# Kernel optimization log

Hardware: AMD Instinct MI355X
Metric: run time of the kernel (lower is better)

The kernel has to match this reference:

```python
import jax, jax.numpy as jnp
import numpy as np

B, T, N, CIN = 8, 12, 883, 3
C, E, H = 64, 10, 8
HD = C // H
TOPK = 48  # int(5 * log2(883))
DIL = [1, 2, 1, 2, 1, 2, 1, 2]
NEG = -9.0e15
L = 8

def _l2norm(v, ax):
    return v / jnp.maximum(jnp.linalg.norm(v, axis=ax, keepdims=True), 1e-12)

def _gelu(v):
    return jax.nn.gelu(v, approximate=False)

def setup_inputs():
    key = jax.random.key(0)
    ks = list(jax.random.split(key, 48))
    it = iter(ks)
    ch0 = jax.random.normal(next(it), (B, T, N))
    ch1 = jax.random.uniform(next(it), (B, T, N))                    # time-of-day in [0,1)
    ch2 = jax.random.randint(next(it), (B, T, N), 0, 7).astype(jnp.float32)  # day-of-week
    x = jnp.stack([ch0, ch1, ch2], axis=-1)
    def row_norm(kk):
        a = jax.random.uniform(kk, (N, N))
        return a / a.sum(axis=1, keepdims=True)
    def w(kk, shape):
        fan_in = shape[-2] if len(shape) >= 2 else shape[-1]
        return (jax.random.normal(kk, shape) * (1.0 / float(np.sqrt(fan_in)))).astype(jnp.float32)
    inp = dict(
        x=x,
        support0=row_norm(next(it)),
        support1=row_norm(next(it)),
        TiD=jax.random.normal(next(it), (288, E)) * 0.1,
        DiW=jax.random.normal(next(it), (7, E)) * 0.1,
        E1=jax.random.normal(next(it), (N, E)) * 0.1,
        E2=jax.random.normal(next(it), (N, E)) * 0.1,
        E3=jax.random.normal(next(it), (N, E)) * 0.1,
        Wx=w(next(it), (T // 2 + 1, E)),
        Wd=w(next(it), (N, 4 * E, E)),
        Wxabs=w(next(it), (E, E)),
        start_w=w(next(it), (CIN, C)), start_b=jnp.zeros((C,)),
        Wq=w(next(it), (L, C, C)), bq=jnp.zeros((L, C)),
        Wk=w(next(it), (L, C, C)), bk=jnp.zeros((L, C)),
        Wv=w(next(it), (L, C, C)), bv=jnp.zeros((L, C)),
        W1=w(next(it), (L, C, 4 * C)), b1=jnp.zeros((L, 4 * C)),
        W2=w(next(it), (L, 4 * C, C)), b2=jnp.zeros((L, C)),
        filt_w=jax.random.normal(next(it), (L, 2, C, C)) * (1.0 / float(np.sqrt(2 * C))),
        filt_b=jnp.zeros((L, C)),
        gate_w=jax.random.normal(next(it), (L, 2, C, C)) * (1.0 / float(np.sqrt(2 * C))),
        gate_b=jnp.zeros((L, C)),
        skip_w=w(next(it), (L, C, 256)), skip_b=jnp.zeros((L, 256)),
        gcn_w=w(next(it), (L, 9 * C, C)), gcn_b=jnp.zeros((L, C)),
        bn_g=jnp.ones((L, C)), bn_b=jnp.zeros((L, C)),
        end1_w=w(next(it), (256, 512)), end1_b=jnp.zeros((512,)),
        end2_w=w(next(it), (512, T)), end2_b=jnp.zeros((T,)),
    )
    return inp

def _graph_gen(xs, T_D, D_W, E3, Wx, Wd, Wxabs):
    # xs: [B,T,N] raw signal channel
    xf = jnp.abs(jnp.fft.rfft(xs, axis=1))                 # [B,F=7,N]
    xf = _l2norm(_l2norm(xf, 1), 2)
    xe = jnp.einsum('btn,td->bnd', xf, Wx)                 # [B,N,E]
    e3 = jnp.broadcast_to(E3[None], (xe.shape[0], N, E))
    xcat = jnp.concatenate([xe, e3, T_D, D_W], axis=2)     # [B,N,4E]
    x1 = jax.nn.relu(jnp.einsum('bnf,nfe->bne', xcat, Wd)) # per-node weight
    mu = x1.mean(axis=(1, 2), keepdims=True)               # LayerNorm over [N,E]
    var = ((x1 - mu) ** 2).mean(axis=(1, 2), keepdims=True)
    x1k = (x1 - mu) / jnp.sqrt(var + 1e-8)
    dew = jnp.einsum('bne,ek->bnk', x1k, Wxabs)
    adp = jax.nn.relu(jnp.einsum('bnk,bmk->bnm', dew, x1)) # [B,N,N]
    _, idx = jax.lax.top_k(adp, TOPK)                      # [B,N,K] per-row topk
    bi = jnp.arange(adp.shape[0])[:, None, None]
    ri = jnp.arange(N)[None, :, None]
    mask = jnp.zeros_like(adp).at[bi, ri, idx].set(1.0)
    return jax.nn.softmax(adp * mask, axis=2)

def reference(x, support0, support1, TiD, DiW, E1, E2, E3, Wx, Wd, Wxabs,
              start_w, start_b, Wq, bq, Wk, bk, Wv, bv, W1, b1, W2, b2,
              filt_w, filt_b, gate_w, gate_b, skip_w, skip_b,
              gcn_w, gcn_b, bn_g, bn_b, end1_w, end1_b, end2_w, end2_b):
    tid = (x[:, -1, :, 1] * 288).astype(jnp.int32)         # [B,N]
    T_D = TiD[tid]                                         # [B,N,E]
    D_W = DiW[x[:, -1, :, 2].astype(jnp.int32)]
    Adap = jax.nn.softmax(jax.nn.relu(E1 @ E2.T), axis=1)
    AD = _graph_gen(x[..., 0], T_D, D_W, E3, Wx, Wd, Wxabs)
    supports = [support0, support1, Adap, AD]

    h = jnp.transpose(x, (0, 3, 2, 1))                     # [B,3,N,T]
    h = jnp.pad(h, ((0, 0), (0, 0), (0, 0), (1, 0)))       # pad to receptive_field=13
    h = jnp.einsum('io,bint->bont', start_w, h) + start_b[None, :, None, None]

    skip = None
    for l in range(L):
        res = h
        # --- causal temporal attention ---
        Xa = jnp.transpose(h, (0, 3, 2, 1))                # [B,Tc,N,C]
        Tc = Xa.shape[1]
        q = _gelu(Xa @ Wq[l] + bq[l]).reshape(-1, Tc, N, H, HD)
        k = _gelu(Xa @ Wk[l] + bk[l]).reshape(-1, Tc, N, H, HD)
        v = _gelu(Xa @ Wv[l] + bv[l]).reshape(-1, Tc, N, H, HD)
        att = jnp.einsum('btnhd,bsnhd->bnhts', q, k) / (HD ** 0.5)
        cmask = jnp.tril(jnp.ones((Tc, Tc), bool))
        att = jax.nn.softmax(jnp.where(cmask, att, NEG), axis=-1)
        o = jnp.einsum('bnhts,bsnhd->bnthd', att, v).reshape(-1, N, Tc, C)
        o = _gelu(o @ W1[l] + b1[l]) @ W2[l] + b2[l]
        h = jnp.transpose(o, (0, 3, 1, 2)) + res           # [B,C,N,Tc]
        # --- gated dilated causal conv (kernel (1,2), dilation d) ---
        d = DIL[l]
        a0, a1 = h[..., :-d], h[..., d:]
        f = jnp.tanh(jnp.einsum('io,bint->bont', filt_w[l, 0], a0)
                     + jnp.einsum('io,bint->bont', filt_w[l, 1], a1)
                     + filt_b[l][None, :, None, None])
        g = jax.nn.sigmoid(jnp.einsum('io,bint->bont', gate_w[l, 0], a0)
                           + jnp.einsum('io,bint->bont', gate_w[l, 1], a1)
                           + gate_b[l][None, :, None, None])
        h = f * g
        s = jnp.einsum('io,bint->bont', skip_w[l], h) + skip_b[l][None, :, None, None]
        skip = s if skip is None else s + skip[..., -s.shape[3]:]
        # --- diffusion graph conv, order 2 over 4 supports ---
        out = [h]
        for a in supports:
            if a.ndim == 3:
                x1 = jnp.einsum('bcvt,bwv->bcwt', h, a)
                x2 = jnp.einsum('bcvt,bwv->bcwt', x1, a)
            else:
                x1 = jnp.einsum('bcvt,vw->bcwt', h, a)
                x2 = jnp.einsum('bcvt,vw->bcwt', x1, a)
            out += [x1, x2]
        hc = jnp.concatenate(out, axis=1)                  # [B,9C,N,Tc']
        h = jnp.einsum('io,bint->bont', gcn_w[l], hc) + gcn_b[l][None, :, None, None]
        h = h + res[..., -h.shape[3]:]
        # --- BatchNorm2d (batch statistics, training-mode normalization) ---
        mu = h.mean(axis=(0, 2, 3), keepdims=True)
        var = ((h - mu) ** 2).mean(axis=(0, 2, 3), keepdims=True)
        h = bn_g[l][None, :, None, None] * (h - mu) / jnp.sqrt(var + 1e-5) \
            + bn_b[l][None, :, None, None]

    out = jax.nn.relu(skip)
    out = jax.nn.relu(jnp.einsum('io,bint->bont', end1_w, out)
                      + end1_b[None, :, None, None])
    out = jnp.einsum('io,bint->bont', end2_w, out) + end2_b[None, :, None, None]
    return out  # [B, out_steps=12, N, 1]
```

## Files before the change

kernel.cpp:

```cpp
#include <hip/hip_runtime.h>
#include <math.h>

#define DIVUP(a,b) (((a)+(b)-1)/(b))

namespace {

constexpr int B=8, T=12, N=883, CIN=3, C=64, E=10, H=8, HD=8, TOPK=48, L=8;
constexpr int SKC=256, F7=7, T13=13;
constexpr int NP=896;

typedef __attribute__((ext_vector_type(8))) short bf16x8;
typedef __attribute__((ext_vector_type(4))) float f32x4;

__device__ __forceinline__ float geluf(float x){ return 0.5f*x*(1.0f+erff(x*0.7071067811865475f)); }
__device__ __forceinline__ float sigmf(float x){ return 1.0f/(1.0f+expf(-x)); }
__device__ __forceinline__ float us2f(unsigned short u){ return __uint_as_float(((unsigned)u)<<16); }
__device__ __forceinline__ unsigned short f2us(float f){
  unsigned x=__float_as_uint(f);
  return (unsigned short)((x + 0x7fffu + ((x>>16)&1u))>>16);
}

template<int KK, int STRIDE, int KW>
__device__ __forceinline__ f32x4 tile_mm(
    const unsigned short* sAh, const unsigned short* sAl,
    const unsigned short* __restrict__ Wh, const unsigned short* __restrict__ Wl,
    int colBase, int lane, f32x4 acc){
  int lr=lane&15, lg=lane>>4;
  #pragma unroll
  for(int k0=0;k0<KK;k0+=32){
    bf16x8 ah=*(const bf16x8*)&sAh[lr*STRIDE+k0+8*lg];
    bf16x8 al=*(const bf16x8*)&sAl[lr*STRIDE+k0+8*lg];
    bf16x8 bh=*(const bf16x8*)&Wh[(size_t)(colBase+lr)*KW+k0+8*lg];
    bf16x8 bl=*(const bf16x8*)&Wl[(size_t)(colBase+lr)*KW+k0+8*lg];
    acc=__builtin_amdgcn_mfma_f32_16x16x32_bf16(ah,bh,acc,0,0,0);
    acc=__builtin_amdgcn_mfma_f32_16x16x32_bf16(ah,bl,acc,0,0,0);
    acc=__builtin_amdgcn_mfma_f32_16x16x32_bf16(al,bh,acc,0,0,0);
  }
  return acc;
}

__global__ void k_dft(const float* __restrict__ x, float* __restrict__ xf){
  int idx = blockIdx.x*256 + threadIdx.x;
  if(idx >= B*F7*N) return;
  int n = idx % N; int f = (idx/N) % F7; int b = idx/(N*F7);
  float re=0.f, im=0.f;
  for(int t=0;t<T;t++){
    float v = x[((size_t)(b*T+t)*N+n)*CIN];
    float ang = -6.283185307179586f * (float)(f*t) / 12.0f;
    re += v*cosf(ang); im += v*sinf(ang);
  }
  xf[idx] = sqrtf(re*re+im*im);
}

__global__ void k_l2f(float* __restrict__ xf){
  int idx = blockIdx.x*256 + threadIdx.x;
  if(idx >= B*N) return;
  int n = idx % N; int b = idx / N;
  float s=0.f;
  for(int f=0;f<F7;f++){ float v=xf[((size_t)b*F7+f)*N+n]; s+=v*v; }
  float inv = 1.0f/fmaxf(sqrtf(s), 1e-12f);
  for(int f=0;f<F7;f++) xf[((size_t)b*F7+f)*N+n] *= inv;
}

__global__ void k_l2n(float* __restrict__ xf){
  int bf = blockIdx.x; int tid = threadIdx.x;
  __shared__ float red[256];
  size_t base = (size_t)bf*N;
  float s=0.f;
  for(int i=tid;i<N;i+=256){ float v=xf[base+i]; s+=v*v; }
  red[tid]=s; __syncthreads();
  for(int k=128;k>0;k>>=1){ if(tid<k) red[tid]+=red[tid+k]; __syncthreads(); }
  float inv = 1.0f/fmaxf(sqrtf(red[0]), 1e-12f);
  __syncthreads();
  for(int i=tid;i<N;i+=256) xf[base+i]*=inv;
}

__global__ void k_x1(const float* __restrict__ x, const float* __restrict__ xf,
                     const float* __restrict__ E3, const float* __restrict__ TiD,
                     const float* __restrict__ DiW, const float* __restrict__ Wx,
                     const float* __restrict__ Wd, float* __restrict__ x1){
  int idx = blockIdx.x*256+threadIdx.x;
  if(idx>=B*N) return;
  int n=idx%N, b=idx/N;
  float xc[40];
  for(int d=0;d<E;d++){
    float a=0.f;
    for(int f=0;f<F7;f++) a += xf[((size_t)b*F7+f)*N+n]*Wx[f*E+d];
    xc[d]=a;
  }
  for(int d=0;d<E;d++) xc[10+d]=E3[n*E+d];
  int ti = (int)(x[((size_t)(b*T+(T-1))*N+n)*CIN+1]*288.0f);
  int dw = (int)(x[((size_t)(b*T+(T-1))*N+n)*CIN+2]);
  for(int d=0;d<E;d++) xc[20+d]=TiD[ti*E+d];
  for(int d=0;d<E;d++) xc[30+d]=DiW[dw*E+d];
  for(int e=0;e<E;e++){
    float a=0.f;
    for(int f=0;f<40;f++) a += xc[f]*Wd[((size_t)n*40+f)*E+e];
    x1[(size_t)idx*E+e]=fmaxf(a,0.f);
  }
}

__global__ void k_lnstats(const float* __restrict__ x1, float* __restrict__ st){
  int b=blockIdx.x, tid=threadIdx.x;
  __shared__ float rs[256], rq[256];
  const int M=N*E;
  float s=0.f,q=0.f;
  for(int i=tid;i<M;i+=256){ float v=x1[(size_t)b*M+i]; s+=v; q+=v*v; }
  rs[tid]=s; rq[tid]=q; __syncthreads();
  for(int k=128;k>0;k>>=1){ if(tid<k){ rs[tid]+=rs[tid+k]; rq[tid]+=rq[tid+k]; } __syncthreads(); }
  if(tid==0){ float mu=rs[0]/M; float var=rq[0]/M-mu*mu; st[b*2]=mu; st[b*2+1]=var; }
}

__global__ void k_dew(const float* __restrict__ x1, const float* __restrict__ st,
                      const float* __restrict__ Wxabs, float* __restrict__ dew){
  int idx=blockIdx.x*256+threadIdx.x;
  if(idx>=B*N) return;
  int b=idx/N;
  float mu=st[b*2], var=st[b*2+1];
  float rs=rsqrtf(var+1e-8f);
  float xk[E];
  for(int e=0;e<E;e++) xk[e]=(x1[(size_t)idx*E+e]-mu)*rs;
  for(int k=0;k<E;k++){
    float a=0.f;
    for(int e=0;e<E;e++) a+=xk[e]*Wxabs[e*E+k];
    dew[(size_t)idx*E+k]=a;
  }
}

__global__ void k_adp(const float* __restrict__ dew, const float* __restrict__ x1,
                      float* __restrict__ adp){
  size_t idx=(size_t)blockIdx.x*256+threadIdx.x;
  if(idx>=(size_t)B*N*N) return;
  int m=(int)(idx%N); int n=(int)((idx/N)%N); int b=(int)(idx/((size_t)N*N));
  const float* dr=dew+((size_t)b*N+n)*E;
  const float* xr=x1+((size_t)b*N+m)*E;
  float a=0.f;
  for(int k=0;k<E;k++) a+=dr[k]*xr[k];
  adp[idx]=fmaxf(a,0.f);
}

__global__ __launch_bounds__(256) void k_topk(const float* __restrict__ adp,
                       unsigned short* __restrict__ ADhi, unsigned short* __restrict__ ADlo){
  int row = blockIdx.x*4 + (threadIdx.x>>6);
  int lane = threadIdx.x & 63;
  const float* rp = adp + (size_t)row*N;
  float v[14];
  #pragma unroll
  for(int j=0;j<14;j++){
    int i = lane + j*64;
    v[j] = (i<N) ? rp[i] : -1.f;
  }
  unsigned sel = 0u;
  float m0 = 0.f;
  for(int k=0;k<TOPK;k++){
    float bv = -2.f; int bi = 1<<20;
    #pragma unroll
    for(int j=0;j<14;j++){
      if(!((sel>>j)&1u) && v[j] > bv){ bv = v[j]; bi = lane + j*64; }
    }
    #pragma unroll
    for(int off=1; off<64; off<<=1){
      float ov = __shfl_xor(bv, off);
      int   oi = __shfl_xor(bi, off);
      if(ov > bv || (ov==bv && oi<bi)){ bv=ov; bi=oi; }
    }
    if(k==0) m0 = bv;
    if((bi&63)==lane) sel |= 1u << (bi>>6);
  }
  float pv[14];
  float ls = 0.f;
  #pragma unroll
  for(int j=0;j<14;j++){
    int i = lane + j*64;
    float p = ((sel>>j)&1u) ? v[j] : 0.f;
    pv[j] = p;
    if(i<N) ls += expf(p - m0);
  }
  #pragma unroll
  for(int off=1; off<64; off<<=1) ls += __shfl_xor(ls, off);
  float invZ = 1.f/ls;
  size_t base = ((size_t)(row/N)*NP + (size_t)(row%N))*NP;
  #pragma unroll
  for(int j=0;j<14;j++){
    int i = lane + j*64;
    if(i<N){
      float f = expf(pv[j]-m0)*invZ;
      unsigned short h=f2us(f);
      ADhi[base+i]=h; ADlo[base+i]=f2us(f-us2f(h));
    }
  }
}

__global__ void k_adap(const float* __restrict__ E1, const float* __restrict__ E2,
                       unsigned short* __restrict__ Mh, unsigned short* __restrict__ Ml){
  int v=blockIdx.x, tid=threadIdx.x;
  __shared__ float rowv[N];
  __shared__ float rv[256];
  float e1[E];
  for(int e=0;e<E;e++) e1[e]=E1[v*E+e];
  for(int j=tid;j<N;j+=256){
    float s=0.f;
    for(int e=0;e<E;e++) s+=e1[e]*E2[j*E+e];
    rowv[j]=fmaxf(s,0.f);
  }
  __syncthreads();
  float lm=-1e30f;
  for(int j=tid;j<N;j+=256) lm=fmaxf(lm,rowv[j]);
  rv[tid]=lm; __syncthreads();
  for(int s=128;s>0;s>>=1){ if(tid<s) rv[tid]=fmaxf(rv[tid],rv[tid+s]); __syncthreads(); }
  float m=rv[0]; __syncthreads();
  float ls=0.f;
  for(int j=tid;j<N;j+=256) ls+=expf(rowv[j]-m);
  rv[tid]=ls; __syncthreads();
  for(int s=128;s>0;s>>=1){ if(tid<s) rv[tid]+=rv[tid+s]; __syncthreads(); }
  float invZ=1.0f/rv[0];
  for(int j=tid;j<N;j+=256){
    float f=expf(rowv[j]-m)*invZ;
    unsigned short h=f2us(f);
    Mh[(size_t)j*NP+v]=h; Ml[(size_t)j*NP+v]=f2us(f-us2f(h));
  }
}

__global__ void k_cvtT(const float* __restrict__ A, unsigned short* __restrict__ Mh,
                       unsigned short* __restrict__ Ml){
  int idx=blockIdx.x*256+threadIdx.x;
  if(idx>=N*N) return;
  int w=idx/N, v=idx%N;
  float f=A[(size_t)v*N+w];
  unsigned short h=f2us(f);
  Mh[(size_t)w*NP+v]=h;
  Ml[(size_t)w*NP+v]=f2us(f-us2f(h));
}

__global__ void k_cvt_qkv(const float* __restrict__ Wq, const float* __restrict__ Wk,
                          const float* __restrict__ Wv,
                          unsigned short* __restrict__ dh, unsigned short* __restrict__ dl){
  int idx=blockIdx.x*256+threadIdx.x;
  if(idx>=L*192*64) return;
  int l=idx/12288, rem=idx%12288, col=rem/64, k=rem%64;
  int mat=col>>6, o=col&63;
  const float* W=(mat==0)?Wq:((mat==1)?Wk:Wv);
  float v=W[(size_t)l*4096 + k*64 + o];
  unsigned short h=f2us(v);
  dh[idx]=h; dl[idx]=f2us(v-us2f(h));
}
__global__ void k_cvt_w1(const float* __restrict__ W1,
                         unsigned short* __restrict__ dh, unsigned short* __restrict__ dl){
  int idx=blockIdx.x*256+threadIdx.x;
  if(idx>=L*256*64) return;
  int l=idx/16384, rem=idx%16384, col=rem/64, k=rem%64;
  float v=W1[(size_t)l*16384 + k*256 + col];
  unsigned short h=f2us(v);
  dh[idx]=h; dl[idx]=f2us(v-us2f(h));
}
__global__ void k_cvt_w2(const float* __restrict__ W2,
                         unsigned short* __restrict__ dh, unsigned short* __restrict__ dl){
  int idx=blockIdx.x*256+threadIdx.x;
  if(idx>=L*64*256) return;
  int l=idx/16384, rem=idx%16384, col=rem/256, k=rem%256;
  float v=W2[(size_t)l*16384 + k*64 + col];
  unsigned short h=f2us(v);
  dh[idx]=h; dl[idx]=f2us(v-us2f(h));
}
__global__ void k_cvt_conv(const float* __restrict__ fw, const float* __restrict__ gw,
                           unsigned short* __restrict__ dh, unsigned short* __restrict__ dl){
  int idx=blockIdx.x*256+threadIdx.x;
  if(idx>=L*128*128) return;
  int l=idx/16384, rem=idx%16384, col=rem/128, k=rem%128;
  int c=col&63, fg=col>>6, tap=k>>6, i=k&63;
  const float* W=fg?gw:fw;
  float v=W[(size_t)l*8192 + tap*4096 + i*64 + c];
  unsigned short h=f2us(v);
  dh[idx]=h; dl[idx]=f2us(v-us2f(h));
}
__global__ void k_cvt_gcn(const float* __restrict__ Wg,
                          unsigned short* __restrict__ dh, unsigned short* __restrict__ dl){
  int idx=blockIdx.x*256+threadIdx.x;
  if(idx>=L*64*576) return;
  int l=idx/36864, rem=idx%36864, o=rem/576, k=rem%576;
  float v=Wg[((size_t)l*576 + k)*64 + o];
  unsigned short h=f2us(v);
  dh[idx]=h; dl[idx]=f2us(v-us2f(h));
}

__global__ void k_zero(float* __restrict__ p, int n){
  int idx=blockIdx.x*256+threadIdx.x;
  if(idx<n) p[idx]=0.f;
}
__global__ void k_zeroUS(unsigned short* __restrict__ p, long long n){
  long long idx=(long long)blockIdx.x*256+threadIdx.x;
  if(idx<n) p[idx]=0;
}

__global__ __launch_bounds__(256) void k_trx(
    const unsigned short* __restrict__ Sh, const unsigned short* __restrict__ Sl,
    unsigned short* __restrict__ Dh, unsigned short* __restrict__ Dl, int M){
  __shared__ unsigned short th[64][66], tl[64][66];
  int b=blockIdx.z;
  int m0=blockIdx.x*64, n0=blockIdx.y*64;
  int tid=threadIdx.x;
  const unsigned short* sbh=Sh + (size_t)b*N*M;
  const unsigned short* sbl=Sl + (size_t)b*N*M;
  for(int idx=tid; idx<64*64; idx+=256){
    int i=idx>>6, j=idx&63;
    int n=n0+i;
    unsigned short vh=0, vl=0;
    if(n<N){
      size_t o=(size_t)n*M + m0+j;
      vh=sbh[o]; vl=sbl[o];
    }
    th[j][i]=vh; tl[j][i]=vl;
  }
  __syncthreads();
  unsigned short* dbh=Dh + (size_t)b*M*NP;
  unsigned short* dbl=Dl + (size_t)b*M*NP;
  for(int idx=tid; idx<64*64; idx+=256){
    int r=idx>>6, cc=idx&63;
    size_t o=(size_t)(m0+r)*NP + n0+cc;
    dbh[o]=th[r][cc]; dbl[o]=tl[r][cc];
  }
}

__global__ void k_start(const float* __restrict__ x, const float* __restrict__ sw,
                        const float* __restrict__ sb, float* __restrict__ h){
  int idx=blockIdx.x*256+threadIdx.x;
  if(idx>=B*N*T13*C) return;
  int c=idx&63; int t=(idx>>6)%T13; int n=(idx/(64*T13))%N; int b=idx/(64*T13*N);
  float a=sb[c];
  if(t>0){
    size_t xb=((size_t)(b*T+(t-1))*N+n)*CIN;
    for(int i=0;i<CIN;i++) a += sw[i*C+c]*x[xb+i];
  }
  h[idx]=a;
}

template<int TC, int D>
__global__ __launch_bounds__(256) void k_attconv(const float* __restrict__ hin,
  const unsigned short* __restrict__ Wqkvh, const unsigned short* __restrict__ Wqkvl,
  const unsigned short* __restrict__ W1h,   const unsigned short* __restrict__ W1l,
  const unsigned short* __restrict__ W2h,   const unsigned short* __restrict__ W2l,
  const unsigned short* __restrict__ Wch,   const unsigned short* __restrict__ Wcl,
  const float* __restrict__ bq, const float* __restrict__ bk, const float* __restrict__ bv,
  const float* __restrict__ b1, const float* __restrict__ b2,
  const float* __restrict__ fb, const float* __restrict__ gb,
  const float* __restrict__ skw, const float* __restrict__ skb,
  unsigned short* __restrict__ hThi, unsigned short* __restrict__ hTlo,
  float* __restrict__ skipacc){
  constexpr int TN = TC - D;
  int bn=blockIdx.x; int tid=threadIdx.x;
  int n=bn%N, b=bn/N;
  int lane=tid&63, wid=tid>>6;
  int lr=lane&15, lg=lane>>4;
  __shared__ __align__(16) float sxa[16*64];
  __shared__ __align__(16) float sq [16*64];
  __shared__ __align__(16) float sk [16*64];
  __shared__ __align__(16) float sv [16*64];
  __shared__ __align__(16) unsigned short sA1h[16*72], sA1l[16*72];
  __shared__ __align__(16) unsigned short sA2h[16*264], sA2l[16*264];
  __shared__ __align__(16) float sfg[16*128];

  const float* hp = hin + (size_t)bn*TC*64;
  for(int idx=tid; idx<TC*64; idx+=256){
    int t=idx>>6, c=idx&63;
    float v=hp[idx];
    sxa[idx]=v;
    unsigned short h=f2us(v);
    sA1h[t*72+c]=h; sA1l[t*72+c]=f2us(v-us2f(h));
  }
  for(int idx=tid; idx<(16-TC)*64; idx+=256){
    int t=TC+(idx>>6), c=idx&63;
    sxa[t*64+c]=0.f; sA1h[t*72+c]=0; sA1l[t*72+c]=0;
  }
  __syncthreads();

  #pragma unroll
  for(int it=0; it<3; ++it){
    int tile=it*4+wid;
    f32x4 acc={0.f,0.f,0.f,0.f};
    acc=tile_mm<64,72,64>(sA1h,sA1l,Wqkvh,Wqkvl,tile*16,lane,acc);
    int col=tile*16+lr; int mat=col>>6, o=col&63;
    const float* bm=(mat==0)?bq:((mat==1)?bk:bv);
    float* dst=(mat==0)?sq:((mat==1)?sk:sv);
    float bias=bm[o];
    #pragma unroll
    for(int r=0;r<4;r++){
      int t=lg*4+r;
      if(t<TC) dst[t*64+o]=geluf(acc[r]+bias);
    }
  }
  __syncthreads();

  if(tid<H*TC){
    int hh=tid/TC, t=tid%TC;
    const float* qr=&sq[t*64+hh*HD];
    float att[TC];
    float m=-1e30f;
    #pragma unroll
    for(int s=0;s<TC;s++){
      float a=0.f;
      #pragma unroll
      for(int d=0;d<HD;d++) a+=qr[d]*sk[s*64+hh*HD+d];
      a*=0.3535533905932738f;
      a=(s<=t)?a:-1e30f;
      att[s]=a; m=fmaxf(m,a);
    }
    float Z=0.f;
    #pragma unroll
    for(int s=0;s<TC;s++){ float e=expf(att[s]-m); att[s]=e; Z+=e; }
    float invZ=1.0f/Z;
    #pragma unroll
    for(int d=0;d<HD;d++){
      float o=0.f;
      #pragma unroll
      for(int s=0;s<TC;s++) o+=att[s]*sv[s*64+hh*HD+d];
      float v=o*invZ;
      unsigned short h=f2us(v);
      sA1h[t*72+hh*8+d]=h; sA1l[t*72+hh*8+d]=f2us(v-us2f(h));
    }
  }
  __syncthreads();

  #pragma unroll
  for(int it=0; it<4; ++it){
    int tile=it*4+wid;
    f32x4 acc={0.f,0.f,0.f,0.f};
    acc=tile_mm<64,72,64>(sA1h,sA1l,W1h,W1l,tile*16,lane,acc);
    int col=tile*16+lr;
    float bias=b1[col];
    #pragma unroll
    for(int r=0;r<4;r++){
      int t=lg*4+r;
      float v=(t<TC)?geluf(acc[r]+bias):0.f;
      unsigned short h=f2us(v);
      sA2h[t*264+col]=h; sA2l[t*264+col]=f2us(v-us2f(h));
    }
  }
  __syncthreads();

  {
    int tile=wid;
    f32x4 acc={0.f,0.f,0.f,0.f};
    acc=tile_mm<256,264,256>(sA2h,sA2l,W2h,W2l,tile*16,lane,acc);
    int col=tile*16+lr;
    float bias=b2[col];
    #pragma unroll
    for(int r=0;r<4;r++){
      int t=lg*4+r;
      if(t<TC) sq[t*64+col]=acc[r]+bias+sxa[t*64+col];
    }
  }
  __syncthreads();

  for(int idx=tid; idx<16*128; idx+=256){
    int t=idx>>7, k=idx&127;
    int c=k&63;
    float v=0.f;
    if(t<TN) v=sq[((k<64)?t:(t+D))*64+c];
    unsigned short h=f2us(v);
    sA2h[t*136+k]=h; sA2l[t*136+k]=f2us(v-us2f(h));
  }
  __syncthreads();

  #pragma unroll
  for(int it=0; it<2; ++it){
    int tile=it*4+wid;
    f32x4 acc={0.f,0.f,0.f,0.f};
    acc=tile_mm<128,136,128>(sA2h,sA2l,Wch,Wcl,tile*16,lane,acc);
    int col=tile*16+lr;
    float bias=(col<64)?fb[col]:gb[col&63];
    #pragma unroll
    for(int r=0;r<4;r++){
      int t=lg*4+r;
      float v=acc[r]+bias;
      sfg[t*128+col]=(col<64)?tanhf(v):sigmf(v);
    }
  }
  __syncthreads();

  if(tid<C) sk[tid]=sfg[(TN-1)*128+tid]*sfg[(TN-1)*128+64+tid];
  __syncthreads();

  {
    float a=skb[tid];
    for(int i=0;i<C;i++) a+=sk[i]*skw[i*SKC+tid];
    skipacc[((size_t)b*SKC+tid)*N+n]+=a;
  }
  size_t obase=(size_t)bn*64*TN;
  for(int idx=tid; idx<TN*64; idx+=256){
    int tt=idx>>6, c=idx&63;
    float v=sfg[tt*128+c]*sfg[tt*128+64+c];
    unsigned short h=f2us(v);
    hThi[obase+idx]=h;
    hTlo[obase+idx]=f2us(v-us2f(h));
  }
}

__global__ __launch_bounds__(256) void k_spatmm(
    const unsigned short* __restrict__ Ah, const unsigned short* __restrict__ Al,
    long long aStride,
    const unsigned short* __restrict__ Xh, const unsigned short* __restrict__ Xl,
    const unsigned short* __restrict__ XTh, const unsigned short* __restrict__ XTl,
    int xT,
    unsigned short* __restrict__ Yh, unsigned short* __restrict__ Yl,
    unsigned short* __restrict__ YTh, unsigned short* __restrict__ YTl,
    int M){
  __shared__ unsigned short sAh[64*40];
  __shared__ unsigned short sAl[64*40];
  __shared__ unsigned short sXh[64*40];
  __shared__ unsigned short sXl[64*40];
  int b=blockIdx.z;
  const unsigned short* Abh=Ah+(size_t)b*aStride;
  const unsigned short* Abl=Al+(size_t)b*aStride;
  int tid=threadIdx.x;
  int w0=blockIdx.x*64, c0=blockIdx.y*64;
  int lane=tid&63, wid=tid>>6;
  int wr=wid>>1, wc=wid&1;
  int lr=lane&15, lg=lane>>4;
  f32x4 acc[2][2];
  #pragma unroll
  for(int j=0;j<2;j++){
    #pragma unroll
    for(int i=0;i<2;i++){ acc[j][i][0]=0.f; acc[j][i][1]=0.f; acc[j][i][2]=0.f; acc[j][i][3]=0.f; }
  }
  const int ar=tid>>2, akb=(tid&3)*8;
  const int xk=tid>>3, xcb=(tid&7)*8;
  const int xkx=xk ^ (8*((xcb>>3)&3));
  for(int k0=0;k0<N;k0+=32){
    {
      uint4 qh=*(const uint4*)&Abh[(size_t)(w0+ar)*NP + k0+akb];
      uint4 ql=*(const uint4*)&Abl[(size_t)(w0+ar)*NP + k0+akb];
      *(uint4*)&sAh[ar*40+akb]=qh;
      *(uint4*)&sAl[ar*40+akb]=ql;
    }
    if(xT){
      const unsigned short* Xbth=XTh+(size_t)b*M*NP;
      const unsigned short* Xbtl=XTl+(size_t)b*M*NP;
      uint4 qh=*(const uint4*)&Xbth[(size_t)(c0+ar)*NP + k0+akb];
      uint4 ql=*(const uint4*)&Xbtl[(size_t)(c0+ar)*NP + k0+akb];
      *(uint4*)&sXh[ar*40+akb]=qh;
      *(uint4*)&sXl[ar*40+akb]=ql;
    }else{
      const unsigned short* Xbh=Xh+(size_t)b*N*M;
      const unsigned short* Xbl=Xl+(size_t)b*N*M;
      uint4 qh={0,0,0,0}, ql={0,0,0,0};
      if(k0+xk<N){
        qh=*(const uint4*)&Xbh[(size_t)(k0+xk)*M + c0+xcb];
        ql=*(const uint4*)&Xbl[(size_t)(k0+xk)*M + c0+xcb];
      }
      unsigned short uh[8], ul[8];
      uh[0]=(unsigned short)(qh.x&0xffff); uh[1]=(unsigned short)(qh.x>>16);
      uh[2]=(unsigned short)(qh.y&0xffff); uh[3]=(unsigned short)(qh.y>>16);
      uh[4]=(unsigned short)(qh.z&0xffff); uh[5]=(unsigned short)(qh.z>>16);
      uh[6]=(unsigned short)(qh.w&0xffff); uh[7]=(unsigned short)(qh.w>>16);
      ul[0]=(unsigned short)(ql.x&0xffff); ul[1]=(unsigned short)(ql.x>>16);
      ul[2]=(unsigned short)(ql.y&0xffff); ul[3]=(unsigned short)(ql.y>>16);
      ul[4]=(unsigned short)(ql.z&0xffff); ul[5]=(unsigned short)(ql.z>>16);
      ul[6]=(unsigned short)(ql.w&0xffff); ul[7]=(unsigned short)(ql.w>>16);
      #pragma unroll
      for(int j=0;j<8;j++){
        sXh[(xcb+j)*40+xkx]=uh[j];
        sXl[(xcb+j)*40+xkx]=ul[j];
      }
    }
    __syncthreads();
    bf16x8 a_h[2], a_l[2], x_h[2], x_l[2];
    #pragma unroll
    for(int j=0;j<2;j++){
      int r=32*wr+16*j+lr;
      a_h[j]=*(const bf16x8*)&sAh[r*40+8*lg];
      a_l[j]=*(const bf16x8*)&sAl[r*40+8*lg];
    }
    #pragma unroll
    for(int i=0;i<2;i++){
      int cc=32*wc+16*i+lr;
      int g = xT ? lg : (lg ^ ((cc>>3)&3));
      x_h[i]=*(const bf16x8*)&sXh[cc*40+8*g];
      x_l[i]=*(const bf16x8*)&sXl[cc*40+8*g];
    }
    #pragma unroll
    for(int j=0;j<2;j++){
      #pragma unroll
      for(int i=0;i<2;i++){
        acc[j][i]=__builtin_amdgcn_mfma_f32_16x16x32_bf16(a_h[j],x_h[i],acc[j][i],0,0,0);
        acc[j][i]=__builtin_amdgcn_mfma_f32_16x16x32_bf16(a_h[j],x_l[i],acc[j][i],0,0,0);
        acc[j][i]=__builtin_amdgcn_mfma_f32_16x16x32_bf16(a_l[j],x_h[i],acc[j][i],0,0,0);
      }
    }
    __syncthreads();
  }
  #pragma unroll
  for(int j=0;j<2;j++){
    int rbase=w0+32*wr+16*j+lg*4;
    #pragma unroll
    for(int i=0;i<2;i++){
      int col=c0+32*wc+16*i+lr;
      unsigned short hh[4], ll[4];
      #pragma unroll
      for(int r=0;r<4;r++){
        float v=acc[j][i][r];
        hh[r]=f2us(v);
        ll[r]=f2us(v-us2f(hh[r]));
      }
      #pragma unroll
      for(int r=0;r<4;r++){
        int row=rbase+r;
        if(row<N){
          size_t o=((size_t)b*N+row)*M+col;
          Yh[o]=hh[r]; Yl[o]=ll[r];
        }
      }
      if(YTh){
        size_t o=(size_t)b*M*NP + (size_t)col*NP + rbase;
        ushort4 ph; ph.x=hh[0]; ph.y=hh[1]; ph.z=hh[2]; ph.w=hh[3];
        ushort4 pl; pl.x=ll[0]; pl.y=ll[1]; pl.z=ll[2]; pl.w=ll[3];
        *(ushort4*)&YTh[o]=ph;
        *(ushort4*)&YTl[o]=pl;
      }
    }
  }
}

template<int TN, int FIRST>
__global__ __launch_bounds__(256) void k_gcnmm(
    const unsigned short* __restrict__ S0h, const unsigned short* __restrict__ S0l,
    const unsigned short* __restrict__ S1h, const unsigned short* __restrict__ S1l,
    const unsigned short* __restrict__ S2h, const unsigned short* __restrict__ S2l,
    const unsigned short* __restrict__ Wbh, const unsigned short* __restrict__ Wbl,
    int kOff,
    const float* __restrict__ gb, const float* __restrict__ res,
    float* __restrict__ acc, int Tc){
  constexpr int SL=64*TN;
  constexpr int NS=FIRST?3:2;
  constexpr int KK=NS*64;
  __shared__ unsigned short sAh[64*40], sAl[64*40];
  int bn0=blockIdx.x*4;
  int tid=threadIdx.x, lane=tid&63, wid=tid>>6;
  int lr=lane&15, lg=lane>>4;
  f32x4 a4[4];
  #pragma unroll
  for(int rt=0;rt<4;rt++){ a4[rt][0]=0.f; a4[rt][1]=0.f; a4[rt][2]=0.f; a4[rt][3]=0.f; }
  const int ar=tid>>2, akb=(tid&3)*8;
  const int ani=ar>>4, att_=ar&15;
  #pragma unroll
  for(int kc=0; kc<KK/32; ++kc){
    int k0=kc*32; int j=k0>>6; int i0=k0&63;
    const unsigned short* sh=(j==0)?S0h:((j==1)?S1h:S2h);
    const unsigned short* sl=(j==0)?S0l:((j==1)?S1l:S2l);
    uint4 qh={0,0,0,0}, ql={0,0,0,0};
    if(att_<TN){
      size_t o=(size_t)(bn0+ani)*SL + att_*64 + i0 + akb;
      qh=*(const uint4*)&sh[o]; ql=*(const uint4*)&sl[o];
    }
    *(uint4*)&sAh[ar*40+akb]=qh;
    *(uint4*)&sAl[ar*40+akb]=ql;
    __syncthreads();
    bf16x8 bh=*(const bf16x8*)&Wbh[(size_t)(wid*16+lr)*576 + kOff + k0 + 8*lg];
    bf16x8 bl=*(const bf16x8*)&Wbl[(size_t)(wid*16+lr)*576 + kOff + k0 + 8*lg];
    #pragma unroll
    for(int rt=0;rt<4;rt++){
      bf16x8 ah=*(const bf16x8*)&sAh[(rt*16+lr)*40+8*lg];
      bf16x8 al=*(const bf16x8*)&sAl[(rt*16+lr)*40+8*lg];
      a4[rt]=__builtin_amdgcn_mfma_f32_16x16x32_bf16(ah,bh,a4[rt],0,0,0);
      a4[rt]=__builtin_amdgcn_mfma_f32_16x16x32_bf16(ah,bl,a4[rt],0,0,0);
      a4[rt]=__builtin_amdgcn_mfma_f32_16x16x32_bf16(al,bh,a4[rt],0,0,0);
    }
    __syncthreads();
  }
  int o=wid*16+lr;
  #pragma unroll
  for(int rt=0;rt<4;rt++){
    int bn=bn0+rt;
    #pragma unroll
    for(int r=0;r<4;r++){
      int t2=lg*4+r;
      if(t2<TN){
        size_t oi=((size_t)bn*TN + t2)*64 + o;
        float v=a4[rt][r];
        if(FIRST){
          v += gb[o] + res[((size_t)bn*Tc + (Tc-TN) + t2)*64 + o];
          acc[oi]=v;
        }else{
          acc[oi]+=v;
        }
      }
    }
  }
}

__global__ __launch_bounds__(256) void k_bnstats1(const float* __restrict__ h,
                                                  float* __restrict__ part, int R){
  int tid=threadIdx.x;
  int c=tid&63, rg=tid>>6;
  float s=0.f,q=0.f;
  for(int r=blockIdx.x*4+rg; r<R; r+=1024){
    float v=h[(size_t)r*64+c];
    s+=v; q+=v*v;
  }
  __shared__ float ls[256], lq[256];
  ls[tid]=s; lq[tid]=q; __syncthreads();
  if(rg==0){
    s=ls[c]+ls[64+c]+ls[128+c]+ls[192+c];
    q=lq[c]+lq[64+c]+lq[128+c]+lq[192+c];
    part[blockIdx.x*128+c]=s;
    part[blockIdx.x*128+64+c]=q;
  }
}
__global__ __launch_bounds__(256) void k_bnstats2(const float* __restrict__ part,
                                                  float* __restrict__ st, int R){
  int tid=threadIdx.x;
  int c=tid&63, g=tid>>6;
  float s=0.f,q=0.f;
  for(int p=g;p<256;p+=4){ s+=part[p*128+c]; q+=part[p*128+64+c]; }
  __shared__ float ls[256], lq[256];
  ls[tid]=s; lq[tid]=q; __syncthreads();
  if(g==0){
    s=ls[c]+ls[64+c]+ls[128+c]+ls[192+c];
    q=lq[c]+lq[64+c]+lq[128+c]+lq[192+c];
    float mu=s/R;
    float var=q/R-mu*mu;
    st[c]=mu; st[64+c]=rsqrtf(var+1e-5f);
  }
}

__global__ void k_bnapply(float* __restrict__ h, const float* __restrict__ st,
                          const float* __restrict__ g, const float* __restrict__ bb, int total){
  int idx=blockIdx.x*256+threadIdx.x;
  if(idx>=total) return;
  int c=idx&63;
  float v=h[idx];
  h[idx]=(v-st[c])*st[64+c]*g[c]+bb[c];
}

__global__ void k_head(const float* __restrict__ skipacc, const float* __restrict__ W1,
  const float* __restrict__ b1, const float* __restrict__ W2, const float* __restrict__ b2,
  float* __restrict__ out){
  int gid=blockIdx.x; int tid=threadIdx.x;
  int n=gid%N; int b=gid/N;
  __shared__ float s[SKC];
  __shared__ float hid[512];
  if(tid<SKC){
    float v=skipacc[((size_t)b*SKC+tid)*N+n];
    s[tid]=fmaxf(v,0.f);
  }
  __syncthreads();
  {
    float a=b1[tid];
    for(int i=0;i<SKC;i++) a+=s[i]*W1[(size_t)i*512+tid];
    hid[tid]=fmaxf(a,0.f);
  }
  __syncthreads();
  if(tid<T){
    float a=b2[tid];
    for(int j=0;j<512;j++) a+=hid[j]*W2[(size_t)j*T+tid];
    out[((size_t)b*T+tid)*N+n]=a;
  }
}

struct Ctx {
  const float *bq,*bk,*bv,*b1,*b2,*filt_b,*gate_b,*skip_w,*skip_b,*gcn_b,*bn_g,*bn_b;
  const unsigned short *qkvTh,*qkvTl,*w1Th,*w1Tl,*w2Th,*w2Tl,*cvTh,*cvTl,*wgh,*wgl;
  const unsigned short* matH[4];
  const unsigned short* matL[4];
  long long matStride[4];
  float *pH,*pAlt,*skipacc,*bnst,*bnpart;
  unsigned short *hThi,*hTlo,*Phi,*Plo,*Qhi,*Qlo;
  unsigned short *hTth,*hTtl,*PTh,*PTl;
  hipStream_t stream;
};

template<int TC, int D>
void run_layer(Ctx& c, int l, bool last){
  constexpr int TN=TC-D;
  k_attconv<TC,D><<<B*N,256,0,c.stream>>>(c.pH,
    c.qkvTh+(size_t)l*12288, c.qkvTl+(size_t)l*12288,
    c.w1Th+(size_t)l*16384,  c.w1Tl+(size_t)l*16384,
    c.w2Th+(size_t)l*16384,  c.w2Tl+(size_t)l*16384,
    c.cvTh+(size_t)l*16384,  c.cvTl+(size_t)l*16384,
    c.bq+(size_t)l*C, c.bk+(size_t)l*C, c.bv+(size_t)l*C,
    c.b1+(size_t)l*4*C, c.b2+(size_t)l*C,
    c.filt_b+(size_t)l*C, c.gate_b+(size_t)l*C,
    c.skip_w+(size_t)l*C*SKC, c.skip_b+(size_t)l*SKC,
    c.hThi, c.hTlo, c.skipacc);
  if(!last){
    int M=C*TN, nMB=M/64;
    const unsigned short* Wh=c.wgh+(size_t)l*36864;
    const unsigned short* Wl=c.wgl+(size_t)l*36864;
    dim3 sg(DIVUP(N,64), nMB, B);
    k_trx<<<dim3(M/64,DIVUP(NP,64),B),256,0,c.stream>>>(c.hThi,c.hTlo, c.hTth,c.hTtl, M);
    for(int s=0;s<4;s++){
      k_spatmm<<<sg,256,0,c.stream>>>(c.matH[s],c.matL[s],c.matStride[s],
          nullptr,nullptr, c.hTth,c.hTtl, 1,
          c.Phi,c.Plo, c.PTh,c.PTl, M);
      if(c.PTh){
        k_spatmm<<<sg,256,0,c.stream>>>(c.matH[s],c.matL[s],c.matStride[s],
            nullptr,nullptr, c.PTh,c.PTl, 1,
            c.Qhi,c.Qlo, nullptr,nullptr, M);
      }else{
        k_spatmm<<<sg,256,0,c.stream>>>(c.matH[s],c.matL[s],c.matStride[s],
            c.Phi,c.Plo, nullptr,nullptr, 0,
            c.Qhi,c.Qlo, nullptr,nullptr, M);
      }
      if(s==0){
        k_gcnmm<TN,1><<<(B*N)/4,256,0,c.stream>>>(
            c.hThi,c.hTlo, c.Phi,c.Plo, c.Qhi,c.Qlo,
            Wh,Wl, 0, c.gcn_b+(size_t)l*C, c.pH, c.pAlt, TC);
      }else{
        k_gcnmm<TN,0><<<(B*N)/4,256,0,c.stream>>>(
            c.Phi,c.Plo, c.Qhi,c.Qlo, nullptr,nullptr,
            Wh,Wl, (1+2*s)*64, nullptr, nullptr, c.pAlt, TC);
      }
    }
    int R=B*N*TN;
    k_bnstats1<<<256,256,0,c.stream>>>(c.pAlt, c.bnpart, R);
    k_bnstats2<<<1,256,0,c.stream>>>(c.bnpart, c.bnst, R);
    k_bnapply<<<DIVUP(R*64,256),256,0,c.stream>>>(c.pAlt, c.bnst,
      c.bn_g+(size_t)l*C, c.bn_b+(size_t)l*C, R*64);
    float* tmp=c.pH; c.pH=c.pAlt; c.pAlt=tmp;
  }
}

}

extern "C" void kernel_launch(void* const* d_in, const int* in_sizes, int n_in,
                              void* d_out, int out_size, void* d_ws, size_t ws_size,
                              hipStream_t stream){
  (void)in_sizes; (void)n_in;
  const float* x      =(const float*)d_in[0];
  const float* sup0   =(const float*)d_in[1];
  const float* sup1   =(const float*)d_in[2];
  const float* TiD    =(const float*)d_in[3];
  const float* DiW    =(const float*)d_in[4];
  const float* E1     =(const float*)d_in[5];
  const float* E2     =(const float*)d_in[6];
  const float* E3     =(const float*)d_in[7];
  const float* Wx     =(const float*)d_in[8];
  const float* Wd     =(const float*)d_in[9];
  const float* Wxabs  =(const float*)d_in[10];
  const float* start_w=(const float*)d_in[11];
  const float* start_b=(const float*)d_in[12];
  const float* Wq     =(const float*)d_in[13];
  const float* Wk     =(const float*)d_in[15];
  const float* Wv     =(const float*)d_in[17];
  const float* W1     =(const float*)d_in[19];
  const float* W2     =(const float*)d_in[21];
  const float* filt_w =(const float*)d_in[23];
  const float* gate_w =(const float*)d_in[25];
  const float* gcn_w  =(const float*)d_in[29];

  Ctx c;
  c.bq=(const float*)d_in[14];
  c.bk=(const float*)d_in[16];
  c.bv=(const float*)d_in[18];
  c.b1=(const float*)d_in[20];
  c.b2=(const float*)d_in[22];
  c.filt_b=(const float*)d_in[24];
  c.gate_b=(const float*)d_in[26];
  c.skip_w=(const float*)d_in[27]; c.skip_b=(const float*)d_in[28];
  c.gcn_b =(const float*)d_in[30];
  c.bn_g  =(const float*)d_in[31]; c.bn_b  =(const float*)d_in[32];
  const float* end1_w =(const float*)d_in[33];
  const float* end1_b =(const float*)d_in[34];
  const float* end2_w =(const float*)d_in[35];
  const float* end2_b =(const float*)d_in[36];
  c.stream=stream;

  size_t off=0;
  auto allocF=[&](size_t nf)->float*{
    nf=(nf+3)&~(size_t)3;
    float* p=(float*)((char*)d_ws+off);
    off += nf*sizeof(float);
    return p;
  };
  auto allocU=[&](size_t nu)->unsigned short*{
    nu=(nu+7)&~(size_t)7;
    unsigned short* p=(unsigned short*)((char*)d_ws+off);
    off += nu*sizeof(unsigned short);
    return p;
  };
  const size_t HMAX =(size_t)B*C*N*T13;
  const size_t XSZ  =(size_t)B*C*N*12;
  const size_t XTSZ =(size_t)768*NP*B;
  const size_t SUPP =(size_t)NP*NP;
  const size_t ADSZ =(size_t)B*NP*NP;

  float* xf     = allocF((size_t)B*F7*N);
  float* gx1    = allocF((size_t)B*N*E);
  float* gdew   = allocF((size_t)B*N*E);
  float* gst    = allocF(16);
  c.bnst        = allocF(2*C);
  c.bnpart      = allocF(256*128);
  float* adp    = allocF((size_t)B*N*N);
  c.pH          = allocF(HMAX);
  c.pAlt        = allocF(HMAX);
  c.skipacc     = allocF((size_t)B*SKC*N);
  unsigned short* matRegion=(unsigned short*)((char*)d_ws+off);
  unsigned short* s0h = allocU(SUPP);
  unsigned short* s0l = allocU(SUPP);
  unsigned short* s1h = allocU(SUPP);
  unsigned short* s1l = allocU(SUPP);
  unsigned short* aph = allocU(SUPP);
  unsigned short* apl = allocU(SUPP);
  unsigned short* adh = allocU(ADSZ);
  unsigned short* adl = allocU(ADSZ);
  long long matRegionN = (long long)(( (unsigned short*)((char*)d_ws+off) ) - matRegion);
  c.hThi = allocU(XSZ);  c.hTlo = allocU(XSZ);
  c.Phi  = allocU(XSZ);  c.Plo  = allocU(XSZ);
  c.Qhi  = allocU(XSZ);  c.Qlo  = allocU(XSZ);
  unsigned short* qkvTh = allocU((size_t)L*12288);
  unsigned short* qkvTl = allocU((size_t)L*12288);
  unsigned short* w1Th  = allocU((size_t)L*16384);
  unsigned short* w1Tl  = allocU((size_t)L*16384);
  unsigned short* w2Th  = allocU((size_t)L*16384);
  unsigned short* w2Tl  = allocU((size_t)L*16384);
  unsigned short* cvTh  = allocU((size_t)L*16384);
  unsigned short* cvTl  = allocU((size_t)L*16384);
  unsigned short* wgh   = allocU((size_t)L*36864);
  unsigned short* wgl   = allocU((size_t)L*36864);
  if(off > ws_size){
    k_zero<<<DIVUP(out_size,256),256,0,stream>>>((float*)d_out, out_size);
    return;
  }
  c.hTth = (unsigned short*)adp;
  c.hTtl = c.hTth + XTSZ;
  {
    size_t save=off;
    c.PTh = allocU(XTSZ);
    c.PTl = allocU(XTSZ);
    if(off > ws_size){ c.PTh=nullptr; c.PTl=nullptr; off=save; }
  }
  c.qkvTh=qkvTh; c.qkvTl=qkvTl; c.w1Th=w1Th; c.w1Tl=w1Tl;
  c.w2Th=w2Th; c.w2Tl=w2Tl; c.cvTh=cvTh; c.cvTl=cvTl;
  c.wgh=wgh; c.wgl=wgl;
  c.matH[0]=s0h; c.matL[0]=s0l; c.matStride[0]=0;
  c.matH[1]=s1h; c.matL[1]=s1l; c.matStride[1]=0;
  c.matH[2]=aph; c.matL[2]=apl; c.matStride[2]=0;
  c.matH[3]=adh; c.matL[3]=adl; c.matStride[3]=(long long)NP*NP;

  k_zeroUS<<<(int)DIVUP(matRegionN,256),256,0,stream>>>(matRegion, matRegionN);
  k_cvt_qkv <<<DIVUP(L*192*64,256),256,0,stream>>>(Wq,Wk,Wv,qkvTh,qkvTl);
  k_cvt_w1  <<<DIVUP(L*256*64,256),256,0,stream>>>(W1,w1Th,w1Tl);
  k_cvt_w2  <<<DIVUP(L*64*256,256),256,0,stream>>>(W2,w2Th,w2Tl);
  k_cvt_conv<<<DIVUP(L*128*128,256),256,0,stream>>>(filt_w,gate_w,cvTh,cvTl);
  k_cvt_gcn <<<DIVUP(L*64*576,256),256,0,stream>>>(gcn_w,wgh,wgl);
  k_dft <<<DIVUP(B*F7*N,256),256,0,stream>>>(x, xf);
  k_l2f <<<DIVUP(B*N,256),256,0,stream>>>(xf);
  k_l2n <<<B*F7,256,0,stream>>>(xf);
  k_x1  <<<DIVUP(B*N,256),256,0,stream>>>(x, xf, E3, TiD, DiW, Wx, Wd, gx1);
  k_lnstats<<<B,256,0,stream>>>(gx1, gst);
  k_dew <<<DIVUP(B*N,256),256,0,stream>>>(gx1, gst, Wxabs, gdew);
  k_adp <<<DIVUP(B*N*N,256),256,0,stream>>>(gdew, gx1, adp);
  k_topk<<<(B*N)/4,256,0,stream>>>(adp, adh, adl);
  k_adap<<<N,256,0,stream>>>(E1, E2, aph, apl);
  k_cvtT<<<DIVUP(N*N,256),256,0,stream>>>(sup0, s0h, s0l);
  k_cvtT<<<DIVUP(N*N,256),256,0,stream>>>(sup1, s1h, s1l);

  k_zero<<<DIVUP(B*SKC*N,256),256,0,stream>>>(c.skipacc, B*SKC*N);
  k_start<<<DIVUP(B*N*T13*C,256),256,0,stream>>>(x, start_w, start_b, c.pH);

  run_layer<13,1>(c,0,false);
  run_layer<12,2>(c,1,false);
  run_layer<10,1>(c,2,false);
  run_layer< 9,2>(c,3,false);
  run_layer< 7,1>(c,4,false);
  run_layer< 6,2>(c,5,false);
  run_layer< 4,1>(c,6,false);
  run_layer< 3,2>(c,7,true);

  k_head<<<B*N,512,0,stream>>>(c.skipacc, end1_w, end1_b, end2_w, end2_b, (float*)d_out);
}
```

Measured before the change: 5.684 ms.

## Fold BatchNorm apply into consumers and make skip accumulator node-major

Removes the standalone BatchNorm apply pass. The normalization is now applied on load in the next layer's attention/conv kernel and in the residual read of the first GCN matmul, which saves a full read-modify-write of the activation tensor per layer. The skip accumulator layout changes to [B*N, 256] so each block writes a contiguous row, and the first layer assigns instead of adding, which drops the zeroing kernel. The cost is extra per-element arithmetic and parameter loads inside the consumer kernels.

Result: no change. 5.656 ms (-0.5%).

```diff
diff --git a/kernel.cpp b/kernel.cpp
--- a/kernel.cpp
+++ b/kernel.cpp
@@ -344,11 +344,11 @@
   const float* __restrict__ b1, const float* __restrict__ b2,
   const float* __restrict__ fb, const float* __restrict__ gb,
   const float* __restrict__ skw, const float* __restrict__ skb,
+  const float* __restrict__ bnst, const float* __restrict__ bng, const float* __restrict__ bnb,
   unsigned short* __restrict__ hThi, unsigned short* __restrict__ hTlo,
-  float* __restrict__ skipacc){
+  float* __restrict__ skipacc, int first){
   constexpr int TN = TC - D;
   int bn=blockIdx.x; int tid=threadIdx.x;
-  int n=bn%N, b=bn/N;
   int lane=tid&63, wid=tid>>6;
   int lr=lane&15, lg=lane>>4;
   __shared__ __align__(16) float sxa[16*64];
@@ -363,6 +363,7 @@
   for(int idx=tid; idx<TC*64; idx+=256){
     int t=idx>>6, c=idx&63;
     float v=hp[idx];
+    if(bng) v=(v-bnst[c])*bnst[64+c]*bng[c]+bnb[c];
     sxa[idx]=v;
     unsigned short h=f2us(v);
     sA1h[t*72+c]=h; sA1l[t*72+c]=f2us(v-us2f(h));
@@ -483,7 +484,8 @@
   {
     float a=skb[tid];
     for(int i=0;i<C;i++) a+=sk[i]*skw[i*SKC+tid];
-    skipacc[((size_t)b*SKC+tid)*N+n]+=a;
+    size_t so_=(size_t)bn*SKC+tid;
+    if(first) skipacc[so_]=a; else skipacc[so_]+=a;
   }
   size_t obase=(size_t)bn*64*TN;
   for(int idx=tid; idx<TN*64; idx+=256){
@@ -628,6 +630,7 @@
     const unsigned short* __restrict__ Wbh, const unsigned short* __restrict__ Wbl,
     int kOff,
     const float* __restrict__ gb, const float* __restrict__ res,
+    const float* __restrict__ bnst, const float* __restrict__ bng, const float* __restrict__ bnb,
     float* __restrict__ acc, int Tc){
   constexpr int SL=64*TN;
   constexpr int NS=FIRST?3:2;
@@ -677,7 +680,9 @@
         size_t oi=((size_t)bn*TN + t2)*64 + o;
         float v=a4[rt][r];
         if(FIRST){
-          v += gb[o] + res[((size_t)bn*Tc + (Tc-TN) + t2)*64 + o];
+          float rr=res[((size_t)bn*Tc + (Tc-TN) + t2)*64 + o];
+          if(bng) rr=(rr-bnst[o])*bnst[64+o]*bng[o]+bnb[o];
+          v += gb[o] + rr;
           acc[oi]=v;
         }else{
           acc[oi]+=v;
@@ -722,15 +727,6 @@
   }
 }
 
-__global__ void k_bnapply(float* __restrict__ h, const float* __restrict__ st,
-                          const float* __restrict__ g, const float* __restrict__ bb, int total){
-  int idx=blockIdx.x*256+threadIdx.x;
-  if(idx>=total) return;
-  int c=idx&63;
-  float v=h[idx];
-  h[idx]=(v-st[c])*st[64+c]*g[c]+bb[c];
-}
-
 __global__ void k_head(const float* __restrict__ skipacc, const float* __restrict__ W1,
   const float* __restrict__ b1, const float* __restrict__ W2, const float* __restrict__ b2,
   float* __restrict__ out){
@@ -739,7 +735,7 @@
   __shared__ float s[SKC];
   __shared__ float hid[512];
   if(tid<SKC){
-    float v=skipacc[((size_t)b*SKC+tid)*N+n];
+    float v=skipacc[(size_t)gid*SKC+tid];
     s[tid]=fmaxf(v,0.f);
   }
   __syncthreads();
@@ -771,6 +767,9 @@
 template<int TC, int D>
 void run_layer(Ctx& c, int l, bool last){
   constexpr int TN=TC-D;
+  const float* ibnst=(l>0)?c.bnst:nullptr;
+  const float* ibng =(l>0)?(c.bn_g+(size_t)(l-1)*C):nullptr;
+  const float* ibnb =(l>0)?(c.bn_b+(size_t)(l-1)*C):nullptr;
   k_attconv<TC,D><<<B*N,256,0,c.stream>>>(c.pH,
     c.qkvTh+(size_t)l*12288, c.qkvTl+(size_t)l*12288,
     c.w1Th+(size_t)l*16384,  c.w1Tl+(size_t)l*16384,
@@ -780,7 +779,8 @@
     c.b1+(size_t)l*4*C, c.b2+(size_t)l*C,
     c.filt_b+(size_t)l*C, c.gate_b+(size_t)l*C,
     c.skip_w+(size_t)l*C*SKC, c.skip_b+(size_t)l*SKC,
-    c.hThi, c.hTlo, c.skipacc);
+    ibnst, ibng, ibnb,
+    c.hThi, c.hTlo, c.skipacc, l==0?1:0);
   if(!last){
     int M=C*TN, nMB=M/64;
     const unsigned short* Wh=c.wgh+(size_t)l*36864;
@@ -803,18 +803,18 @@
       if(s==0){
         k_gcnmm<TN,1><<<(B*N)/4,256,0,c.stream>>>(
             c.hThi,c.hTlo, c.Phi,c.Plo, c.Qhi,c.Qlo,
-            Wh,Wl, 0, c.gcn_b+(size_t)l*C, c.pH, c.pAlt, TC);
+            Wh,Wl, 0, c.gcn_b+(size_t)l*C, c.pH,
+            ibnst, ibng, ibnb, c.pAlt, TC);
       }else{
         k_gcnmm<TN,0><<<(B*N)/4,256,0,c.stream>>>(
             c.Phi,c.Plo, c.Qhi,c.Qlo, nullptr,nullptr,
-            Wh,Wl, (1+2*s)*64, nullptr, nullptr, c.pAlt, TC);
+            Wh,Wl, (1+2*s)*64, nullptr, nullptr,
+            nullptr,nullptr,nullptr, c.pAlt, TC);
       }
     }
     int R=B*N*TN;
     k_bnstats1<<<256,256,0,c.stream>>>(c.pAlt, c.bnpart, R);
     k_bnstats2<<<1,256,0,c.stream>>>(c.bnpart, c.bnst, R);
-    k_bnapply<<<DIVUP(R*64,256),256,0,c.stream>>>(c.pAlt, c.bnst,
-      c.bn_g+(size_t)l*C, c.bn_b+(size_t)l*C, R*64);
     float* tmp=c.pH; c.pH=c.pAlt; c.pAlt=tmp;
   }
 }
@@ -892,7 +892,7 @@
   float* adp    = allocF((size_t)B*N*N);
   c.pH          = allocF(HMAX);
   c.pAlt        = allocF(HMAX);
-  c.skipacc     = allocF((size_t)B*SKC*N);
+  c.skipacc     = allocF((size_t)B*N*SKC);
   unsigned short* matRegion=(unsigned short*)((char*)d_ws+off);
   unsigned short* s0h = allocU(SUPP);
   unsigned short* s0l = allocU(SUPP);
@@ -954,7 +954,6 @@
   k_cvtT<<<DIVUP(N*N,256),256,0,stream>>>(sup0, s0h, s0l);
   k_cvtT<<<DIVUP(N*N,256),256,0,stream>>>(sup1, s1h, s1l);
 
-  k_zero<<<DIVUP(B*SKC*N,256),256,0,stream>>>(c.skipacc, B*SKC*N);
   k_start<<<DIVUP(B*N*T13*C,256),256,0,stream>>>(x, start_w, start_b, c.pH);
 
   run_layer<13,1>(c,0,false);
```
